# Kernel tuning notes

Hardware: AMD Instinct MI355X
Metric: run time of the kernel (lower is better)

Reference implementation:

```python
import jax, jax.numpy as jnp
import numpy as np

# RootMLP architecture constants (data_size=16, width=64, depth=2, in=1, out=2*data)
DATA = 16
WIDTH = 64
OUT = 2 * DATA
LAYER_SHAPES = [(WIDTH, 1), (WIDTH,), (WIDTH, WIDTH), (WIDTH,), (OUT, WIDTH), (OUT,)]
SIZES = [int(np.prod(s)) for s in LAYER_SHAPES]
OFFS = np.cumsum([0] + SIZES).tolist()
LATENT = OFFS[-1]  # 6368


def _mlp_apply(thet, x):
    # Unflatten latent vector into MLP weights (order: W0,b0,W1,b1,W2,b2) and run it.
    W0 = thet[OFFS[0]:OFFS[1]].reshape(WIDTH, 1)
    b0 = thet[OFFS[1]:OFFS[2]]
    W1 = thet[OFFS[2]:OFFS[3]].reshape(WIDTH, WIDTH)
    b1 = thet[OFFS[3]:OFFS[4]]
    W2 = thet[OFFS[4]:OFFS[5]].reshape(OUT, WIDTH)
    b2 = thet[OFFS[5]:OFFS[6]]
    h = jax.nn.relu(W0 @ x + b0)
    h = jax.nn.relu(W1 @ h + b1)
    return W2 @ h + b2  # (OUT,)


def setup_inputs() -> dict:
    key = jax.random.key(0)
    k1, k2, k3, k4 = jax.random.split(key, 4)
    batch, T = 8, 64
    xs = jax.random.normal(k1, (batch, T, DATA), dtype=jnp.float32)
    ts = jnp.tile(jnp.linspace(0.0, 1.0, T, dtype=jnp.float32), (batch, 1))
    # A initialized as identity in the source; tiny noise keeps the recurrence non-trivial yet stable.
    A = jnp.eye(LATENT, dtype=jnp.float32) + 1e-4 * jax.random.normal(k2, (LATENT, LATENT), dtype=jnp.float32)
    B = 0.01 * jax.random.normal(k3, (LATENT, DATA + 1), dtype=jnp.float32)
    theta0 = 0.05 * jax.random.normal(k4, (LATENT,), dtype=jnp.float32)
    return {"xs": xs, "ts": ts, "A": A, "B": B, "theta0": theta0}


def reference(xs, ts, A, B, theta0):
    # xs: (batch, T, DATA); ts: (batch, T)
    def forward(xs_, ts_):
        def f(carry, inp):
            thet, x_hat, x_prev, t_prev = carry
            x_true, t_curr = inp  # x_true: (DATA,), t_curr: (1,)
            delta_t = t_curr - t_prev
            # forcing_prob = 1.0  ->  bernoulli(key, 1.0) is always True -> teacher forcing
            x_t = x_true
            # time_as_channel=True: prepend time to both current and previous inputs
            xt_c = jnp.concatenate([t_curr, x_t])
            xp_c = jnp.concatenate([t_prev, x_prev])
            thet_next = A @ thet + B @ (xt_c - xp_c)
            root_in = t_curr + delta_t  # (1,)
            out = _mlp_apply(thet_next, root_in)  # (2*DATA,)
            mean = jnp.tanh(out[:DATA])
            std = jax.nn.softplus(jnp.tanh(out[DATA:]))  # apply_tanh_uncertainty=True
            x_next = jnp.concatenate([mean, std])
            # carry update per source: new x_hat = mean, new x_prev = old x_hat
            return (thet_next, mean, x_hat, t_curr), x_next

        init = (theta0, xs_[0], xs_[0], -ts_[1:2])
        _, ys = jax.lax.scan(f, init, (xs_, ts_[:, None]))
        return ys  # (T, 2*DATA)

    return jax.vmap(forward)(xs, ts)
```

## Files before the change

kernel.cpp:

```cpp
#include <hip/hip_runtime.h>
#include <hip/hip_bf16.h>
#include <cmath>

#define LATENT 6368
#define TSTEPS 64
#define NDATA 16
#define NPANEL 398
#define KSPLIT 8
#define NCHUNK 199
#define CPS 25
#define NTILE (NPANEL*KSPLIT)
#define KBLK 796
#define AGENT __HIP_MEMORY_SCOPE_AGENT

typedef __attribute__((ext_vector_type(8))) short short8v;
typedef __attribute__((ext_vector_type(4))) float floatx4;

__device__ __forceinline__ unsigned short f2bf(float x) {
    union { float f; unsigned u; } c; c.f = x;
    unsigned r = (c.u + 0x7FFFu + ((c.u >> 16) & 1u)) >> 16;
    return (unsigned short)r;
}
__device__ __forceinline__ float bf2f(unsigned short h) {
    union { unsigned u; float f; } c; c.u = ((unsigned)h) << 16; return c.f;
}

__device__ __forceinline__ unsigned long long ld64c(const void* p) {
    return __hip_atomic_load((const unsigned long long*)p, __ATOMIC_RELAXED, AGENT);
}
__device__ __forceinline__ short8v ldT16c(const unsigned short* p) {
    union { short8v v; unsigned long long q[2]; } r;
    r.q[0] = ld64c(p);
    r.q[1] = ld64c(p + 4);
    return r.v;
}
__device__ __forceinline__ float ldfc(const float* p) {
    return __hip_atomic_load(p, __ATOMIC_RELAXED, AGENT);
}
__device__ __forceinline__ void stfc(float* p, float v) {
    __hip_atomic_store(p, v, __ATOMIC_RELAXED, AGENT);
}
__device__ __forceinline__ void stu16c(unsigned short* p, unsigned short v) {
    __hip_atomic_store(p, v, __ATOMIC_RELAXED, AGENT);
}

__global__ __launch_bounds__(64) void row_scale(const float* __restrict__ A,
                                                float* __restrict__ S) {
    int row = blockIdx.x;
    int lane = threadIdx.x;
    const float* Ar = A + (size_t)row * LATENT;
    float m = 0.f;
    for (int i = 0; i < 25; ++i) {
        int idx = i * 256 + lane * 4;
        if (idx + 4 <= LATENT) {
            float4 v = *reinterpret_cast<const float4*>(Ar + idx);
            float a0 = v.x - (idx + 0 == row ? 1.f : 0.f);
            float a1 = v.y - (idx + 1 == row ? 1.f : 0.f);
            float a2 = v.z - (idx + 2 == row ? 1.f : 0.f);
            float a3 = v.w - (idx + 3 == row ? 1.f : 0.f);
            m = fmaxf(m, fmaxf(fmaxf(fabsf(a0), fabsf(a1)), fmaxf(fabsf(a2), fabsf(a3))));
        }
    }
#pragma unroll
    for (int o = 32; o; o >>= 1) m = fmaxf(m, __shfl_xor(m, o, 64));
    if (lane == 0) S[row] = fmaxf(m, 1e-30f) * (1.0f / 32767.0f);
}

__global__ __launch_bounds__(256) void convert_Eq(const float* __restrict__ A,
                                                  const float* __restrict__ S,
                                                  short* __restrict__ Eq,
                                                  int total) {
    int t = blockIdx.x * 256 + threadIdx.x;
    if (t >= total) return;
    int row = t / KBLK;
    int kb  = t - row * KBLK;
    const float4* src = reinterpret_cast<const float4*>(A + (size_t)row * LATENT + kb * 8);
    float4 v0 = src[0];
    float4 v1 = src[1];
    float v[8] = {v0.x, v0.y, v0.z, v0.w, v1.x, v1.y, v1.z, v1.w};
    int jd = row - kb * 8;
    if (jd >= 0 && jd < 8) v[jd] -= 1.0f;
    float inv = 1.0f / S[row];
    union { short8v s; short q[8]; } o;
#pragma unroll
    for (int j = 0; j < 8; ++j) {
        float qf = rintf(v[j] * inv);
        qf = fminf(fmaxf(qf, -32767.f), 32767.f);
        o.q[j] = (short)qf;
    }
    int p = row >> 4, rowl = row & 15, c = kb >> 2, kgrp = kb & 3;
    int lane = kgrp * 16 + rowl;
    *reinterpret_cast<short8v*>(Eq + ((size_t)(p * NCHUNK + c)) * 512 + lane * 8) = o.s;
}

__global__ __launch_bounds__(256) void init_theta(const float* __restrict__ th0,
                                                  float* __restrict__ T0,
                                                  unsigned short* __restrict__ TTf) {
    int r = blockIdx.x * blockDim.x + threadIdx.x;
    if (r >= LATENT) return;
    float v = th0[r];
#pragma unroll
    for (int b = 0; b < 8; ++b) T0[r * 8 + b] = v;
    unsigned short hb = f2bf(v);
    unsigned short lb = f2bf(v - bf2f(hb));
    int c = r >> 5, kg = (r & 31) >> 3, j = r & 7;
    size_t base = (size_t)c * 512 + kg * 128;
#pragma unroll
    for (int n = 0; n < 8; ++n) {
        stu16c(&TTf[base + n * 8 + j], hb);
        stu16c(&TTf[base + (n + 8) * 8 + j], lb);
    }
}

__device__ void mlp_batch(const float* __restrict__ Tcur, const float* __restrict__ ts,
                          float* __restrict__ mwrite, float* __restrict__ ys,
                          int i, int b, int lane) {
    float tc = ts[b * TSTEPS + i];
    float tp = (i == 0) ? -ts[b * TSTEPS + 1] : ts[b * TSTEPS + i - 1];
    float rin = 2.f * tc - tp;
    float h0 = fmaxf(Tcur[(size_t)lane * 8 + b] * rin + Tcur[(size_t)(64 + lane) * 8 + b], 0.f);
    float h1 = Tcur[(size_t)(4224 + lane) * 8 + b];
#pragma unroll 8
    for (int k = 0; k < 64; ++k)
        h1 += Tcur[(size_t)(128 + lane * 64 + k) * 8 + b] * __shfl(h0, k, 64);
    h1 = fmaxf(h1, 0.f);
    float o = 0.f;
    if (lane < 32) o = Tcur[(size_t)(6336 + lane) * 8 + b];
#pragma unroll 8
    for (int k = 0; k < 64; ++k) {
        float hk = __shfl(h1, k, 64);
        if (lane < 32) o += Tcur[(size_t)(4288 + lane * 64 + k) * 8 + b] * hk;
    }
    if (lane < 32) {
        float z = tanhf(o);
        float res;
        if (lane < 16) { res = z; mwrite[b * NDATA + lane] = z; }
        else           { res = log1pf(expf(z)); }
        ys[(size_t)b * (TSTEPS * 32) + (size_t)i * 32 + lane] = res;
    }
}

__device__ void mlp_batch_coh(const float* __restrict__ Tcur, const float* __restrict__ ts,
                              float* __restrict__ mwrite, float* __restrict__ ys,
                              int i, int b, int lane) {
    float tc = ts[b * TSTEPS + i];
    float tp = (i == 0) ? -ts[b * TSTEPS + 1] : ts[b * TSTEPS + i - 1];
    float rin = 2.f * tc - tp;
    float h0 = fmaxf(ldfc(&Tcur[(size_t)lane * 8 + b]) * rin
                     + ldfc(&Tcur[(size_t)(64 + lane) * 8 + b]), 0.f);
    float h1 = ldfc(&Tcur[(size_t)(4224 + lane) * 8 + b]);
#pragma unroll 8
    for (int k = 0; k < 64; ++k)
        h1 += ldfc(&Tcur[(size_t)(128 + lane * 64 + k) * 8 + b]) * __shfl(h0, k, 64);
    h1 = fmaxf(h1, 0.f);
    float o = 0.f;
    if (lane < 32) o = ldfc(&Tcur[(size_t)(6336 + lane) * 8 + b]);
#pragma unroll 8
    for (int k = 0; k < 64; ++k) {
        float hk = __shfl(h1, k, 64);
        if (lane < 32) o += ldfc(&Tcur[(size_t)(4288 + lane * 64 + k) * 8 + b]) * hk;
    }
    if (lane < 32) {
        float z = tanhf(o);
        float res;
        if (lane < 16) { res = z; stfc(&mwrite[b * NDATA + lane], z); }
        else           { res = log1pf(expf(z)); }
        ys[(size_t)b * (TSTEPS * 32) + (size_t)i * 32 + lane] = res;
    }
}

__device__ __forceinline__ void gsync2(unsigned* grpCnt, unsigned* superCnt,
                                       unsigned* gEpoch, unsigned iter) {
    asm volatile("s_waitcnt vmcnt(0)" ::: "memory");
    __syncthreads();
    if (threadIdx.x == 0) {
        unsigned g = blockIdx.x & 15u;
        unsigned gsz = (g < 8u) ? 13u : 12u;
        unsigned v = __hip_atomic_fetch_add(&grpCnt[g * 32], 1u, __ATOMIC_RELAXED, AGENT);
        if (v == iter * gsz - 1u) {
            unsigned w = __hip_atomic_fetch_add(superCnt, 1u, __ATOMIC_RELAXED, AGENT);
            if (w == iter * 16u - 1u) {
#pragma unroll
                for (int i2 = 0; i2 < 16; ++i2)
                    __hip_atomic_store(&gEpoch[i2 * 32], iter, __ATOMIC_RELAXED, AGENT);
            }
        }
        while (__hip_atomic_load(&gEpoch[g * 32], __ATOMIC_RELAXED, AGENT) < iter)
            __builtin_amdgcn_s_sleep(4);
    }
    __syncthreads();
}

#define COMP2(EA, EB, TP) do {                                                    \
    union { short8v sv; unsigned short us[8]; } HA, LA, HB, LB;                   \
    _Pragma("unroll")                                                             \
    for (int j = 0; j < 8; ++j) {                                                 \
        int qa = (EA)[j], qb = (EB)[j];                                           \
        union { float f; unsigned u; } x0, x1, x2, x3;                            \
        x0.f = (float)(qa >> 8);  HA.us[j] = (unsigned short)(x0.u >> 16);        \
        x1.f = (float)(qa & 255); LA.us[j] = (unsigned short)(x1.u >> 16);        \
        x2.f = (float)(qb >> 8);  HB.us[j] = (unsigned short)(x2.u >> 16);        \
        x3.f = (float)(qb & 255); LB.us[j] = (unsigned short)(x3.u >> 16);        \
    }                                                                             \
    acc1A = __builtin_amdgcn_mfma_f32_16x16x32_bf16(HA.sv, (TP), acc1A, 0, 0, 0); \
    acc2A = __builtin_amdgcn_mfma_f32_16x16x32_bf16(LA.sv, (TP), acc2A, 0, 0, 0); \
    acc1B = __builtin_amdgcn_mfma_f32_16x16x32_bf16(HB.sv, (TP), acc1B, 0, 0, 0); \
    acc2B = __builtin_amdgcn_mfma_f32_16x16x32_bf16(LB.sv, (TP), acc2B, 0, 0, 0); \
} while (0)

#define LDE(P)  (*reinterpret_cast<const short8v*>(P))

__global__ __launch_bounds__(1024, 4) void persistent8(
    const short* __restrict__ Eq, const float* __restrict__ S,
    float* __restrict__ T0buf, float* __restrict__ T1buf,
    unsigned short* __restrict__ TTA, unsigned short* __restrict__ TTB,
    float* __restrict__ mb,
    const float* __restrict__ Bmat, const float* __restrict__ xs,
    const float* __restrict__ ts, float* __restrict__ ys,
    unsigned* grpCnt, unsigned* superCnt, unsigned* gEpoch)
{
    __shared__ float red[16][2][16][16];
    __shared__ float ush[17][8];
    int tid = threadIdx.x, blk = blockIdx.x;
    int wave = tid >> 6, lane = tid & 63;
    int rowl = lane & 15, kgrp = lane >> 4;
    int cs = (wave < 7) ? wave * 13 : 91 + (wave - 7) * 12;
    int nch = (wave < 7) ? 13 : 12;
    int panelA = blk * 2;
    unsigned iter = 0;
    for (int s = 0; s < TSTEPS; ++s) {
        const float* Tc = (s & 1) ? T1buf : T0buf;
        float* Tn       = (s & 1) ? T0buf : T1buf;
        const unsigned short* TTc = (s & 1) ? TTB : TTA;
        unsigned short* TTn       = (s & 1) ? TTA : TTB;
        float* mwrite = mb + (s & 1) * 128;
        const float* mread = mb + ((s & 1) ^ 1) * 128;
        if (blk < 199) {
            if (tid < 136) {
                int b = tid & 7, j = tid >> 3;
                float tc = ts[b * TSTEPS + s];
                float tp = (s == 0) ? -ts[b * TSTEPS + 1] : ts[b * TSTEPS + s - 1];
                float val;
                if (j == 0) val = tc - tp;
                else {
                    int d = j - 1;
                    float xp = (s < 2) ? xs[(b * TSTEPS) * NDATA + d]
                                       : ldfc(&mread[b * NDATA + d]);
                    val = xs[(b * TSTEPS + s) * NDATA + d] - xp;
                }
                ush[j][b] = val;
            }
            floatx4 acc1A = {0.f,0.f,0.f,0.f}, acc2A = {0.f,0.f,0.f,0.f};
            floatx4 acc1B = {0.f,0.f,0.f,0.f}, acc2B = {0.f,0.f,0.f,0.f};
            const short* epA = Eq + ((size_t)(panelA * NCHUNK + cs)) * 512 + lane * 8;
            const short* epB = epA + (size_t)NCHUNK * 512;
            const unsigned short* tq = TTc + (size_t)cs * 512 + lane * 8;
            short8v a0 = LDE(epA),        a1 = LDE(epA + 512),
                    a2 = LDE(epA + 1024), a3 = LDE(epA + 1536);
            short8v b0 = LDE(epB),        b1 = LDE(epB + 512),
                    b2 = LDE(epB + 1024), b3 = LDE(epB + 1536);
            short8v t0 = ldT16c(tq),        t1 = ldT16c(tq + 512),
                    t2 = ldT16c(tq + 1024), t3 = ldT16c(tq + 1536);
            int c = 0;
            for (; c + 8 <= nch; c += 4) {
                COMP2(a0, b0, t0); a0 = LDE(epA + 2048); b0 = LDE(epB + 2048); t0 = ldT16c(tq + 2048);
                COMP2(a1, b1, t1); a1 = LDE(epA + 2560); b1 = LDE(epB + 2560); t1 = ldT16c(tq + 2560);
                COMP2(a2, b2, t2); a2 = LDE(epA + 3072); b2 = LDE(epB + 3072); t2 = ldT16c(tq + 3072);
                COMP2(a3, b3, t3); a3 = LDE(epA + 3584); b3 = LDE(epB + 3584); t3 = ldT16c(tq + 3584);
                epA += 2048; epB += 2048; tq += 2048;
            }
            COMP2(a0, b0, t0); COMP2(a1, b1, t1); COMP2(a2, b2, t2); COMP2(a3, b3, t3);
            for (int k2 = 4; c + k2 < nch; ++k2) {
                a0 = LDE(epA + k2 * 512); b0 = LDE(epB + k2 * 512); t0 = ldT16c(tq + k2 * 512);
                COMP2(a0, b0, t0);
            }
#pragma unroll
            for (int r = 0; r < 4; ++r) {
                red[wave][0][kgrp * 4 + r][rowl] = 256.f * acc1A[r] + acc2A[r];
                red[wave][1][kgrp * 4 + r][rowl] = 256.f * acc1B[r] + acc2B[r];
            }
            __syncthreads();
            if (tid < 256) {
                int m32 = tid >> 3, n = tid & 7;
                int ph = m32 >> 4, m = m32 & 15;
                float sum = 0.f;
#pragma unroll
                for (int w = 0; w < 16; ++w)
                    sum += red[w][ph][m][n] + red[w][ph][m][n + 8];
                int r = blk * 32 + m32;
                float val = ldfc(&Tc[r * 8 + n]) + S[r] * sum;
                const float* Brow = Bmat + r * 17;
#pragma unroll
                for (int j = 0; j < 17; ++j) val += Brow[j] * ush[j][n];
                stfc(&Tn[r * 8 + n], val);
                unsigned short hb = f2bf(val);
                int kg = m32 >> 3, j2 = m32 & 7;
                size_t tb = (size_t)blk * 512 + kg * 128;
                stu16c(&TTn[tb + n * 8 + j2], hb);
                stu16c(&TTn[tb + (n + 8) * 8 + j2], f2bf(val - bf2f(hb)));
            }
        } else {
            if (s >= 1 && wave < 8)
                mlp_batch_coh(Tc, ts, mwrite, ys, s - 1, wave, lane);
        }
        ++iter; gsync2(grpCnt, superCnt, gEpoch, iter);
    }
    if (blk == 199 && wave < 8)
        mlp_batch_coh(T0buf, ts, mb, ys, TSTEPS - 1, wave, lane);
}

template<bool USE_E>
__global__ __launch_bounds__(128) void partial_kernel(
    const short* __restrict__ Eq, const float* __restrict__ S,
    const float* __restrict__ Af,
    const unsigned short* __restrict__ TTc,
    float* __restrict__ P)
{
    int blk = blockIdx.x;
    int p  = blk >> 3;
    int si = blk & 7;
    int tid = threadIdx.x;
    int wave = tid >> 6;
    int lane = tid & 63;
    int rowl = lane & 15;
    int kgrp = lane >> 4;
    int row = p * 16 + rowl;
    int c0 = si * CPS;
    int c1 = c0 + CPS; if (c1 > NCHUNK) c1 = NCHUNK;
    int nch = c1 - c0;
    int half = (nch + 1) >> 1;
    int csw = c0 + wave * half;
    int cew = csw + half; if (cew > c1) cew = c1;
    floatx4 acc1 = {0.f, 0.f, 0.f, 0.f};
    floatx4 acc2 = {0.f, 0.f, 0.f, 0.f};
    for (int c = csw; c < cew; ++c) {
        int k = c * 32 + kgrp * 8;
        short8v ehf, elf;
        if (USE_E) {
            short8v ev = *reinterpret_cast<const short8v*>(
                Eq + ((size_t)(p * NCHUNK + c)) * 512 + lane * 8);
            union { short8v sv; unsigned short us[8]; } EH, EL;
#pragma unroll
            for (int j = 0; j < 8; ++j) {
                int q = ev[j];
                union { float f; unsigned u; } ch2, cl2;
                ch2.f = (float)(q >> 8);
                cl2.f = (float)(q & 255);
                EH.us[j] = (unsigned short)(ch2.u >> 16);
                EL.us[j] = (unsigned short)(cl2.u >> 16);
            }
            ehf = EH.sv; elf = EL.sv;
        } else {
            const float* ap = Af + (size_t)row * LATENT + k;
            float v[8];
#pragma unroll
            for (int j = 0; j < 8; ++j) v[j] = ap[j];
            int jd = row - k;
            if (jd >= 0 && jd < 8) v[jd] -= 1.0f;
            union { short8v sv; unsigned short us[8]; } ch, cl;
#pragma unroll
            for (int j = 0; j < 8; ++j) {
                unsigned short hb = f2bf(v[j]);
                ch.us[j] = hb;
                cl.us[j] = f2bf(v[j] - bf2f(hb));
            }
            ehf = ch.sv; elf = cl.sv;
        }
        short8v tpf = *reinterpret_cast<const short8v*>(TTc + (size_t)c * 512 + lane * 8);
        acc1 = __builtin_amdgcn_mfma_f32_16x16x32_bf16(ehf, tpf, acc1, 0, 0, 0);
        acc2 = __builtin_amdgcn_mfma_f32_16x16x32_bf16(elf, tpf, acc2, 0, 0, 0);
    }
    __shared__ float red[2][16][16];
#pragma unroll
    for (int r = 0; r < 4; ++r)
        red[wave][kgrp * 4 + r][rowl] = USE_E ? (256.f * acc1[r] + acc2[r])
                                              : (acc1[r] + acc2[r]);
    __syncthreads();
    int nn = tid & 15;
    if (nn < 8) {
        for (int mm = tid >> 4; mm < 16; mm += 8) {
            float s2 = red[0][mm][nn] + red[0][mm][nn + 8]
                     + red[1][mm][nn] + red[1][mm][nn + 8];
            if (USE_E) s2 *= S[p * 16 + mm];
            P[((size_t)(p * 8 + si) * 16 + mm) * 8 + nn] = s2;
        }
    }
}

__global__ __launch_bounds__(256) void combine_kernel(
    const float* __restrict__ P,
    const float* __restrict__ Tcur,
    float* __restrict__ Tnxt,
    unsigned short* __restrict__ TTn,
    const float* __restrict__ Bmat,
    const float* __restrict__ xs,
    const float* __restrict__ ts,
    const float* __restrict__ mread,
    float* __restrict__ mwrite,
    float* __restrict__ ys,
    int s, int do_matvec, int do_mlp)
{
    int tid = threadIdx.x;
    if ((int)blockIdx.x < 199) {
        if (!do_matvec) return;
        __shared__ float u[17][8];
        if (tid < 136) {
            int b = tid & 7;
            int j = tid >> 3;
            float tc = ts[b * TSTEPS + s];
            float tp = (s == 0) ? -ts[b * TSTEPS + 1] : ts[b * TSTEPS + s - 1];
            float val;
            if (j == 0) val = tc - tp;
            else {
                int d = j - 1;
                float xp = (s < 2) ? xs[(b * TSTEPS) * NDATA + d] : mread[b * NDATA + d];
                val = xs[(b * TSTEPS + s) * NDATA + d] - xp;
            }
            u[j][b] = val;
        }
        __syncthreads();
        int idx = blockIdx.x * 256 + tid;
        int r = idx >> 3;
        int n = idx & 7;
        int pp = r >> 4, mm = r & 15;
        const float* Pb = P + ((size_t)pp * 8) * 128 + mm * 8 + n;
        float sum = 0.f;
#pragma unroll
        for (int si = 0; si < KSPLIT; ++si) sum += Pb[si * 128];
        float val = Tcur[r * 8 + n] + sum;
        const float* Brow = Bmat + r * 17;
#pragma unroll
        for (int j = 0; j < 17; ++j) val += Brow[j] * u[j][n];
        Tnxt[r * 8 + n] = val;
        unsigned short hb = f2bf(val);
        int c2 = r >> 5, kg = (r & 31) >> 3, j2 = r & 7;
        size_t tb = (size_t)c2 * 512 + kg * 128;
        TTn[tb + n * 8 + j2] = hb;
        TTn[tb + (n + 8) * 8 + j2] = f2bf(val - bf2f(hb));
    } else {
        if (!do_mlp) return;
        int w = tid >> 6, lane = tid & 63;
        for (int it = 0; it < 2; ++it)
            mlp_batch(Tcur, ts, mwrite, ys, s - 1, w * 2 + it, lane);
    }
}

extern "C" void kernel_launch(void* const* d_in, const int* in_sizes, int n_in,
                              void* d_out, int out_size, void* d_ws, size_t ws_size,
                              hipStream_t stream) {
    const float* xs  = (const float*)d_in[0];
    const float* ts  = (const float*)d_in[1];
    const float* A   = (const float*)d_in[2];
    const float* Bm  = (const float*)d_in[3];
    const float* th0 = (const float*)d_in[4];
    float* ys = (float*)d_out;

    char* ws = (char*)d_ws;
    size_t off = 0;
    auto alloc = [&](size_t bytes) {
        void* p = ws + off;
        off += (bytes + 255) & ~(size_t)255;
        return p;
    };
    float* T0 = (float*)alloc((size_t)LATENT * 8 * sizeof(float));
    float* T1 = (float*)alloc((size_t)LATENT * 8 * sizeof(float));
    unsigned short* TTA = (unsigned short*)alloc((size_t)16 * LATENT * 2);
    unsigned short* TTB = (unsigned short*)alloc((size_t)16 * LATENT * 2);
    float* mb = (float*)alloc(2 * 8 * 16 * sizeof(float));
    float* P  = (float*)alloc((size_t)NTILE * 128 * sizeof(float));
    float* S  = (float*)alloc((size_t)LATENT * sizeof(float));
    unsigned* bar = (unsigned*)alloc(8192);
    unsigned* grpCnt   = bar;
    unsigned* superCnt = bar + 512;
    unsigned* gEpoch   = bar + 544;
    size_t Ebytes = (size_t)NPANEL * NCHUNK * 512 * 2;
    bool useE = (off + Ebytes + 512) <= ws_size;
    short* Eq = nullptr;
    if (useE) {
        Eq = (short*)alloc(Ebytes);
        row_scale<<<dim3(LATENT), dim3(64), 0, stream>>>(A, S);
        int nthr = LATENT * KBLK;
        convert_Eq<<<dim3((nthr + 255) / 256), dim3(256), 0, stream>>>(A, S, Eq, nthr);
    }
    init_theta<<<dim3((LATENT + 255) / 256), dim3(256), 0, stream>>>(th0, T0, TTA);

    hipError_t coop = hipErrorUnknown;
    if (useE) {
        hipMemsetAsync(bar, 0, 8192, stream);
        void* kargs[] = {
            (void*)&Eq, (void*)&S, (void*)&T0, (void*)&T1,
            (void*)&TTA, (void*)&TTB, (void*)&mb, (void*)&Bm, (void*)&xs,
            (void*)&ts, (void*)&ys, (void*)&grpCnt, (void*)&superCnt, (void*)&gEpoch };
        coop = hipLaunchCooperativeKernel((void*)persistent8,
                                          dim3(200), dim3(1024), kargs, 0, stream);
    }
    if (coop != hipSuccess) {
        float* T[2] = {T0, T1};
        unsigned short* TT[2] = {TTA, TTB};
        for (int s = 0; s <= TSTEPS; ++s) {
            int cur = s & 1, nxt = cur ^ 1;
            float* mwrite = mb + (s & 1) * 128;
            float* mread  = mb + ((s & 1) ^ 1) * 128;
            int dmv = (s < TSTEPS) ? 1 : 0;
            int dml = (s >= 1) ? 1 : 0;
            if (dmv) {
                if (useE)
                    partial_kernel<true><<<dim3(NTILE), dim3(128), 0, stream>>>(
                        Eq, S, A, TT[cur], P);
                else
                    partial_kernel<false><<<dim3(NTILE), dim3(128), 0, stream>>>(
                        Eq, S, A, TT[cur], P);
            }
            combine_kernel<<<dim3(200), dim3(256), 0, stream>>>(
                P, T[cur], T[nxt], TT[nxt],
                Bm, xs, ts, mread, mwrite, ys, s, dmv, dml);
        }
    }
    (void)in_sizes; (void)n_in; (void)out_size;
}
```

Measured before the change: 2.448 ms.

## Use per-step fresh state buffers so theta reads can use plain cached loads

Replaces the ping-pong theta/TT/mean buffers with 65 separate per-timestep slots at descending addresses, so every step reads addresses that were never read before. This lets the persistent kernel drop the relaxed atomic (coherent) loads and use ordinary vector loads, since no stale cache line can exist for a fresh address. It costs a much larger workspace (about 65 copies of state) and relies on caches not holding prefetched lines of not-yet-written slots.

Result: faster. 2.384 ms (-2.6%).

```diff
diff --git a/kernel.cpp b/kernel.cpp
--- a/kernel.cpp
+++ b/kernel.cpp
@@ -12,6 +12,8 @@
 #define NTILE (NPANEL*KSPLIT)
 #define KBLK 796
 #define AGENT __HIP_MEMORY_SCOPE_AGENT
+#define TSTR  51200
+#define TTSTR 102400
 
 typedef __attribute__((ext_vector_type(8))) short short8v;
 typedef __attribute__((ext_vector_type(4))) float floatx4;
@@ -25,18 +27,6 @@
     union { unsigned u; float f; } c; c.u = ((unsigned)h) << 16; return c.f;
 }
 
-__device__ __forceinline__ unsigned long long ld64c(const void* p) {
-    return __hip_atomic_load((const unsigned long long*)p, __ATOMIC_RELAXED, AGENT);
-}
-__device__ __forceinline__ short8v ldT16c(const unsigned short* p) {
-    union { short8v v; unsigned long long q[2]; } r;
-    r.q[0] = ld64c(p);
-    r.q[1] = ld64c(p + 4);
-    return r.v;
-}
-__device__ __forceinline__ float ldfc(const float* p) {
-    return __hip_atomic_load(p, __ATOMIC_RELAXED, AGENT);
-}
 __device__ __forceinline__ void stfc(float* p, float v) {
     __hip_atomic_store(p, v, __ATOMIC_RELAXED, AGENT);
 }
@@ -95,7 +85,7 @@
 
 __global__ __launch_bounds__(256) void init_theta(const float* __restrict__ th0,
                                                   float* __restrict__ T0,
-                                                  unsigned short* __restrict__ TTf) {
+                                                  unsigned short* __restrict__ TT0) {
     int r = blockIdx.x * blockDim.x + threadIdx.x;
     if (r >= LATENT) return;
     float v = th0[r];
@@ -107,8 +97,36 @@
     size_t base = (size_t)c * 512 + kg * 128;
 #pragma unroll
     for (int n = 0; n < 8; ++n) {
-        stu16c(&TTf[base + n * 8 + j], hb);
-        stu16c(&TTf[base + (n + 8) * 8 + j], lb);
+        TT0[base + n * 8 + j] = hb;
+        TT0[base + (n + 8) * 8 + j] = lb;
+    }
+}
+
+__device__ void mlp_batch_rot(const float* __restrict__ Tcur, const float* __restrict__ ts,
+                              float* __restrict__ mwrite, float* __restrict__ ys,
+                              int i, int b, int lane) {
+    float tc = ts[b * TSTEPS + i];
+    float tp = (i == 0) ? -ts[b * TSTEPS + 1] : ts[b * TSTEPS + i - 1];
+    float rin = 2.f * tc - tp;
+    float h0 = fmaxf(Tcur[(size_t)lane * 8 + b] * rin + Tcur[(size_t)(64 + lane) * 8 + b], 0.f);
+    float h1 = Tcur[(size_t)(4224 + lane) * 8 + b];
+#pragma unroll 8
+    for (int k = 0; k < 64; ++k)
+        h1 += Tcur[(size_t)(128 + lane * 64 + k) * 8 + b] * __shfl(h0, k, 64);
+    h1 = fmaxf(h1, 0.f);
+    float o = 0.f;
+    if (lane < 32) o = Tcur[(size_t)(6336 + lane) * 8 + b];
+#pragma unroll 8
+    for (int k = 0; k < 64; ++k) {
+        float hk = __shfl(h1, k, 64);
+        if (lane < 32) o += Tcur[(size_t)(4288 + lane * 64 + k) * 8 + b] * hk;
+    }
+    if (lane < 32) {
+        float z = tanhf(o);
+        float res;
+        if (lane < 16) { res = z; stfc(&mwrite[b * NDATA + lane], z); }
+        else           { res = log1pf(expf(z)); }
+        ys[(size_t)b * (TSTEPS * 32) + (size_t)i * 32 + lane] = res;
     }
 }
 
@@ -140,35 +158,6 @@
     }
 }
 
-__device__ void mlp_batch_coh(const float* __restrict__ Tcur, const float* __restrict__ ts,
-                              float* __restrict__ mwrite, float* __restrict__ ys,
-                              int i, int b, int lane) {
-    float tc = ts[b * TSTEPS + i];
-    float tp = (i == 0) ? -ts[b * TSTEPS + 1] : ts[b * TSTEPS + i - 1];
-    float rin = 2.f * tc - tp;
-    float h0 = fmaxf(ldfc(&Tcur[(size_t)lane * 8 + b]) * rin
-                     + ldfc(&Tcur[(size_t)(64 + lane) * 8 + b]), 0.f);
-    float h1 = ldfc(&Tcur[(size_t)(4224 + lane) * 8 + b]);
-#pragma unroll 8
-    for (int k = 0; k < 64; ++k)
-        h1 += ldfc(&Tcur[(size_t)(128 + lane * 64 + k) * 8 + b]) * __shfl(h0, k, 64);
-    h1 = fmaxf(h1, 0.f);
-    float o = 0.f;
-    if (lane < 32) o = ldfc(&Tcur[(size_t)(6336 + lane) * 8 + b]);
-#pragma unroll 8
-    for (int k = 0; k < 64; ++k) {
-        float hk = __shfl(h1, k, 64);
-        if (lane < 32) o += ldfc(&Tcur[(size_t)(4288 + lane * 64 + k) * 8 + b]) * hk;
-    }
-    if (lane < 32) {
-        float z = tanhf(o);
-        float res;
-        if (lane < 16) { res = z; stfc(&mwrite[b * NDATA + lane], z); }
-        else           { res = log1pf(expf(z)); }
-        ys[(size_t)b * (TSTEPS * 32) + (size_t)i * 32 + lane] = res;
-    }
-}
-
 __device__ __forceinline__ void gsync2(unsigned* grpCnt, unsigned* superCnt,
                                        unsigned* gEpoch, unsigned iter) {
     asm volatile("s_waitcnt vmcnt(0)" ::: "memory");
@@ -210,11 +199,10 @@
 
 #define LDE(P)  (*reinterpret_cast<const short8v*>(P))
 
-__global__ __launch_bounds__(1024, 4) void persistent8(
+__global__ __launch_bounds__(1024, 4) void persistent9(
     const short* __restrict__ Eq, const float* __restrict__ S,
-    float* __restrict__ T0buf, float* __restrict__ T1buf,
-    unsigned short* __restrict__ TTA, unsigned short* __restrict__ TTB,
-    float* __restrict__ mb,
+    float* __restrict__ Tbase, unsigned short* __restrict__ TTbase,
+    float* __restrict__ mbase,
     const float* __restrict__ Bmat, const float* __restrict__ xs,
     const float* __restrict__ ts, float* __restrict__ ys,
     unsigned* grpCnt, unsigned* superCnt, unsigned* gEpoch)
@@ -229,12 +217,12 @@
     int panelA = blk * 2;
     unsigned iter = 0;
     for (int s = 0; s < TSTEPS; ++s) {
-        const float* Tc = (s & 1) ? T1buf : T0buf;
-        float* Tn       = (s & 1) ? T0buf : T1buf;
-        const unsigned short* TTc = (s & 1) ? TTB : TTA;
-        unsigned short* TTn       = (s & 1) ? TTA : TTB;
-        float* mwrite = mb + (s & 1) * 128;
-        const float* mread = mb + ((s & 1) ^ 1) * 128;
+        const float* Tc = Tbase + (size_t)(64 - s) * TSTR;
+        float* Tn       = Tbase + (size_t)(63 - s) * TSTR;
+        const unsigned short* TTc = TTbase + (size_t)(64 - s) * TTSTR;
+        unsigned short* TTn       = TTbase + (size_t)(63 - s) * TTSTR;
+        float* mwrite = mbase + (size_t)(64 - s) * 128;
+        const float* mread = mbase + (size_t)(65 - s) * 128;
         if (blk < 199) {
             if (tid < 136) {
                 int b = tid & 7, j = tid >> 3;
@@ -245,7 +233,7 @@
                 else {
                     int d = j - 1;
                     float xp = (s < 2) ? xs[(b * TSTEPS) * NDATA + d]
-                                       : ldfc(&mread[b * NDATA + d]);
+                                       : mread[b * NDATA + d];
                     val = xs[(b * TSTEPS + s) * NDATA + d] - xp;
                 }
                 ush[j][b] = val;
@@ -259,19 +247,19 @@
                     a2 = LDE(epA + 1024), a3 = LDE(epA + 1536);
             short8v b0 = LDE(epB),        b1 = LDE(epB + 512),
                     b2 = LDE(epB + 1024), b3 = LDE(epB + 1536);
-            short8v t0 = ldT16c(tq),        t1 = ldT16c(tq + 512),
-                    t2 = ldT16c(tq + 1024), t3 = ldT16c(tq + 1536);
+            short8v t0 = LDE(tq),         t1 = LDE(tq + 512),
+                    t2 = LDE(tq + 1024),  t3 = LDE(tq + 1536);
             int c = 0;
             for (; c + 8 <= nch; c += 4) {
-                COMP2(a0, b0, t0); a0 = LDE(epA + 2048); b0 = LDE(epB + 2048); t0 = ldT16c(tq + 2048);
-                COMP2(a1, b1, t1); a1 = LDE(epA + 2560); b1 = LDE(epB + 2560); t1 = ldT16c(tq + 2560);
-                COMP2(a2, b2, t2); a2 = LDE(epA + 3072); b2 = LDE(epB + 3072); t2 = ldT16c(tq + 3072);
-                COMP2(a3, b3, t3); a3 = LDE(epA + 3584); b3 = LDE(epB + 3584); t3 = ldT16c(tq + 3584);
+                COMP2(a0, b0, t0); a0 = LDE(epA + 2048); b0 = LDE(epB + 2048); t0 = LDE(tq + 2048);
+                COMP2(a1, b1, t1); a1 = LDE(epA + 2560); b1 = LDE(epB + 2560); t1 = LDE(tq + 2560);
+                COMP2(a2, b2, t2); a2 = LDE(epA + 3072); b2 = LDE(epB + 3072); t2 = LDE(tq + 3072);
+                COMP2(a3, b3, t3); a3 = LDE(epA + 3584); b3 = LDE(epB + 3584); t3 = LDE(tq + 3584);
                 epA += 2048; epB += 2048; tq += 2048;
             }
             COMP2(a0, b0, t0); COMP2(a1, b1, t1); COMP2(a2, b2, t2); COMP2(a3, b3, t3);
             for (int k2 = 4; c + k2 < nch; ++k2) {
-                a0 = LDE(epA + k2 * 512); b0 = LDE(epB + k2 * 512); t0 = ldT16c(tq + k2 * 512);
+                a0 = LDE(epA + k2 * 512); b0 = LDE(epB + k2 * 512); t0 = LDE(tq + k2 * 512);
                 COMP2(a0, b0, t0);
             }
 #pragma unroll
@@ -288,7 +276,7 @@
                 for (int w = 0; w < 16; ++w)
                     sum += red[w][ph][m][n] + red[w][ph][m][n + 8];
                 int r = blk * 32 + m32;
-                float val = ldfc(&Tc[r * 8 + n]) + S[r] * sum;
+                float val = Tc[r * 8 + n] + S[r] * sum;
                 const float* Brow = Bmat + r * 17;
 #pragma unroll
                 for (int j = 0; j < 17; ++j) val += Brow[j] * ush[j][n];
@@ -301,12 +289,12 @@
             }
         } else {
             if (s >= 1 && wave < 8)
-                mlp_batch_coh(Tc, ts, mwrite, ys, s - 1, wave, lane);
+                mlp_batch_rot(Tc, ts, mwrite, ys, s - 1, wave, lane);
         }
         ++iter; gsync2(grpCnt, superCnt, gEpoch, iter);
     }
     if (blk == 199 && wave < 8)
-        mlp_batch_coh(T0buf, ts, mb, ys, TSTEPS - 1, wave, lane);
+        mlp_batch_rot(Tbase, ts, mbase, ys, TSTEPS - 1, wave, lane);
 }
 
 template<bool USE_E>
@@ -462,11 +450,9 @@
         off += (bytes + 255) & ~(size_t)255;
         return p;
     };
-    float* T0 = (float*)alloc((size_t)LATENT * 8 * sizeof(float));
-    float* T1 = (float*)alloc((size_t)LATENT * 8 * sizeof(float));
-    unsigned short* TTA = (unsigned short*)alloc((size_t)16 * LATENT * 2);
-    unsigned short* TTB = (unsigned short*)alloc((size_t)16 * LATENT * 2);
-    float* mb = (float*)alloc(2 * 8 * 16 * sizeof(float));
+    float* Tbase = (float*)alloc((size_t)65 * TSTR * sizeof(float));
+    unsigned short* TTbase = (unsigned short*)alloc((size_t)65 * TTSTR * 2);
+    float* mbase = (float*)alloc((size_t)66 * 128 * sizeof(float));
     float* P  = (float*)alloc((size_t)NTILE * 128 * sizeof(float));
     float* S  = (float*)alloc((size_t)LATENT * sizeof(float));
     unsigned* bar = (unsigned*)alloc(8192);
@@ -482,25 +468,26 @@
         int nthr = LATENT * KBLK;
         convert_Eq<<<dim3((nthr + 255) / 256), dim3(256), 0, stream>>>(A, S, Eq, nthr);
     }
-    init_theta<<<dim3((LATENT + 255) / 256), dim3(256), 0, stream>>>(th0, T0, TTA);
+    init_theta<<<dim3((LATENT + 255) / 256), dim3(256), 0, stream>>>(
+        th0, Tbase + (size_t)64 * TSTR, TTbase + (size_t)64 * TTSTR);
 
     hipError_t coop = hipErrorUnknown;
     if (useE) {
         hipMemsetAsync(bar, 0, 8192, stream);
         void* kargs[] = {
-            (void*)&Eq, (void*)&S, (void*)&T0, (void*)&T1,
-            (void*)&TTA, (void*)&TTB, (void*)&mb, (void*)&Bm, (void*)&xs,
+            (void*)&Eq, (void*)&S, (void*)&Tbase, (void*)&TTbase,
+            (void*)&mbase, (void*)&Bm, (void*)&xs,
             (void*)&ts, (void*)&ys, (void*)&grpCnt, (void*)&superCnt, (void*)&gEpoch };
-        coop = hipLaunchCooperativeKernel((void*)persistent8,
+        coop = hipLaunchCooperativeKernel((void*)persistent9,
                                           dim3(200), dim3(1024), kargs, 0, stream);
     }
     if (coop != hipSuccess) {
-        float* T[2] = {T0, T1};
-        unsigned short* TT[2] = {TTA, TTB};
+        float* T[2] = {Tbase + (size_t)64 * TSTR, Tbase + (size_t)63 * TSTR};
+        unsigned short* TT[2] = {TTbase + (size_t)64 * TTSTR, TTbase + (size_t)63 * TTSTR};
         for (int s = 0; s <= TSTEPS; ++s) {
             int cur = s & 1, nxt = cur ^ 1;
-            float* mwrite = mb + (s & 1) * 128;
-            float* mread  = mb + ((s & 1) ^ 1) * 128;
+            float* mwrite = mbase + (s & 1) * 128;
+            float* mread  = mbase + ((s & 1) ^ 1) * 128;
             int dmv = (s < TSTEPS) ? 1 : 0;
             int dml = (s >= 1) ? 1 : 0;
             if (dmv) {
```
